# Kernel tuning notes

Measured on AMD Instinct MI355X. Metric: run time of the kernel, lower is better.

The kernel has to match this reference:

```python
import jax, jax.numpy as jnp
import numpy as np

B, S, HID = 2, 2048, 2048
H = 16
HD = HID // H            # 128
HD2 = HD // 2            # 64 (rope dim per head)
LAT = HID // 8           # 256 latent dim
BASE = 10000.0


def _rotary_table(seq_len):
    # inv_freq over rope dim HD2
    inv_freq = 1.0 / (BASE ** (jnp.arange(0, HD2, 2, dtype=jnp.float32) / HD2))  # [HD2//2]
    pos = jnp.arange(seq_len, dtype=jnp.float32)
    sincos = pos[:, None] * inv_freq[None, :]                 # [S, HD2//2]
    return jnp.concatenate([jnp.sin(sincos), jnp.cos(sincos)], axis=-1)  # [S, HD2]


def _apply_rope(x, emb):
    # x: [B, S, H, HD2]; emb: [S, HD2]
    half = HD2 // 2
    x1, x2 = x[..., :half], x[..., half:]
    sin = emb[None, :, None, :half]
    cos = emb[None, :, None, half:]
    return jnp.concatenate([x1 * cos - x2 * sin, x1 * sin + x2 * cos], axis=-1)


def setup_inputs() -> dict:
    key = jax.random.key(0)
    ks = jax.random.split(key, 9)
    s = 0.02
    return {
        "hidden_states": jax.random.normal(ks[0], (B, S, HID), jnp.float32),
        "w_kv_d": jax.random.normal(ks[1], (HID, LAT), jnp.float32) * s,
        "w_q_d": jax.random.normal(ks[2], (HID, LAT), jnp.float32) * s,
        "w_k_u": jax.random.normal(ks[3], (LAT, H * HD2), jnp.float32) * s,
        "w_q_u": jax.random.normal(ks[4], (LAT, H * HD2), jnp.float32) * s,
        "w_v_u": jax.random.normal(ks[5], (LAT, H * HD), jnp.float32) * s,
        "w_rope_k": jax.random.normal(ks[6], (HID, HID // 2), jnp.float32) * s,
        "w_rope_q": jax.random.normal(ks[7], (LAT, HID // 2), jnp.float32) * s,
        "w_o": jax.random.normal(ks[8], (HID, HID), jnp.float32) * s,
    }


def reference(hidden_states, w_kv_d, w_q_d, w_k_u, w_q_u, w_v_u, w_rope_k, w_rope_q, w_o):
    b, s, _ = hidden_states.shape
    kv_d = hidden_states @ w_kv_d            # [B,S,LAT]
    q_d = hidden_states @ w_q_d              # [B,S,LAT]
    k_p = (kv_d @ w_k_u).reshape(b, s, H, HD2)
    q_p = (q_d @ w_q_u).reshape(b, s, H, HD2)
    v = (kv_d @ w_v_u).reshape(b, s, H, HD)
    k_r = (hidden_states @ w_rope_k).reshape(b, s, H, HD2)
    q_r = (q_d @ w_rope_q).reshape(b, s, H, HD2)

    emb = _rotary_table(s)
    k_r = _apply_rope(k_r, emb)
    q_r = _apply_rope(q_r, emb)

    k = jnp.concatenate([k_p, k_r], axis=-1)  # [B,S,H,HD]
    q = jnp.concatenate([q_p, q_r], axis=-1)

    scores = jnp.einsum('bqhd,bkhd->bhqk', q, k) / jnp.sqrt(jnp.float32(HD))
    causal = jnp.tril(jnp.ones((s, s), dtype=bool))
    scores = jnp.where(causal[None, None], scores, jnp.float32(-1e9))
    probs = jax.nn.softmax(scores, axis=-1)
    out = jnp.einsum('bhqk,bkhd->bqhd', probs, v).reshape(b, s, HID)
    return out @ w_o
```

## Files before the change

kernel.cpp:

```cpp
#include <hip/hip_runtime.h>
#include <hip/hip_bf16.h>

#define BB 2
#define SS 2048
#define HID 2048
#define NH 16
#define BS (BB*SS)
#define SCALE 0.088388347648318447f
#define C2LOG 0.12751743f

typedef __bf16 bf16x8 __attribute__((ext_vector_type(8)));
typedef float f32x4 __attribute__((ext_vector_type(4)));
typedef float f32x16 __attribute__((ext_vector_type(16)));
typedef unsigned int uintx2 __attribute__((ext_vector_type(2)));

__device__ __forceinline__ bf16x8 ld_frag(const __hip_bfloat16* p) {
    uint4 u = *reinterpret_cast<const uint4*>(p);
    return __builtin_bit_cast(bf16x8, u);
}
__device__ __forceinline__ void store_c(__hip_bfloat16* C, size_t idx, float v) {
    C[idx] = __float2bfloat16(v);
}
__device__ __forceinline__ void store_c(float* C, size_t idx, float v) {
    C[idx] = v;
}
__device__ __forceinline__ ushort bf_bits(float v) {
    __hip_bfloat16 h = __float2bfloat16(v);
    return *reinterpret_cast<ushort*>(&h);
}

#define GLD16(gp, lp) \
  __builtin_amdgcn_global_load_lds((const __attribute__((address_space(1))) void*)(gp), \
                                   (__attribute__((address_space(3))) void*)(lp), 16, 0, 0)

__global__ __launch_bounds__(256) void convert_kernel(
    const float* __restrict__ src, __hip_bfloat16* __restrict__ dst, int n8)
{
    int i = blockIdx.x * blockDim.x + threadIdx.x;
    if (i >= n8) return;
    float4 a = reinterpret_cast<const float4*>(src)[2 * i];
    float4 b = reinterpret_cast<const float4*>(src)[2 * i + 1];
    ushort u[8] = { bf_bits(a.x), bf_bits(a.y), bf_bits(a.z), bf_bits(a.w),
                    bf_bits(b.x), bf_bits(b.y), bf_bits(b.z), bf_bits(b.w) };
    reinterpret_cast<uint4*>(dst)[i] = *reinterpret_cast<uint4*>(u);
}

__global__ __launch_bounds__(256) void transpose_weights_kernel(
    const float* s0, const float* s1, const float* s2, const float* s3,
    const float* s4, const float* s5, const float* s6, const float* s7,
    __hip_bfloat16* WT1, __hip_bfloat16* WT2, __hip_bfloat16* WT3,
    __hip_bfloat16* WTo)
{
    const float* srcs[8] = { s0, s1, s2, s3, s4, s5, s6, s7 };
    const int Rs[8] = { 2048, 2048, 2048, 256, 256, 256, 256, 2048 };
    const int Cs[8] = { 256, 256, 1024, 1024, 2048, 1024, 1024, 2048 };
    __hip_bfloat16* dsts[8] = {
        WT1, WT1 + (size_t)256 * 2048, WT1 + (size_t)512 * 2048,
        WT2, WT2 + (size_t)1024 * 256,
        WT3, WT3 + (size_t)1024 * 256,
        WTo };
    const int prefix[9] = { 0, 512, 1024, 3072, 3328, 3840, 4096, 4352, 8448 };

    int bid = blockIdx.x;
    int seg = 0;
    #pragma unroll
    for (int i = 0; i < 8; i++) if (bid >= prefix[i + 1]) seg = i + 1;
    int local = bid - prefix[seg];
    int R = Rs[seg], C = Cs[seg];
    int tilesC = C / 32;
    int tr = local / tilesC, tc = local % tilesC;
    int r0 = tr * 32, c0 = tc * 32;
    const float* src = srcs[seg];
    __hip_bfloat16* dst = dsts[seg];

    __shared__ float Ts[32][33];
    int t = threadIdx.x;
    int ty = t >> 5, tx = t & 31;
    #pragma unroll
    for (int k = 0; k < 4; k++) {
        int r = ty + k * 8;
        Ts[r][tx] = src[(size_t)(r0 + r) * C + c0 + tx];
    }
    __syncthreads();
    #pragma unroll
    for (int k = 0; k < 4; k++) {
        int r = ty + k * 8;
        dst[(size_t)(c0 + r) * R + r0 + tx] = __float2bfloat16(Ts[tx][r]);
    }
}

template <typename TC>
__global__ __launch_bounds__(256) void gemm_bt_kernel(
    const __hip_bfloat16* __restrict__ A, int lda,
    const __hip_bfloat16* __restrict__ Bt,
    TC* __restrict__ C0, int ldc0, int sp0, int off0, float cm0,
    TC* __restrict__ C1, int ldc1, int sp1, int off1, float cm1,
    int splitN, int K)
{
    __shared__ alignas(16) __hip_bfloat16 As[128 * 32];
    __shared__ alignas(16) __hip_bfloat16 Bs[128 * 32];

    const int bn = blockIdx.x * 128;
    const int bm = blockIdx.y * 128;
    const int t = threadIdx.x;
    const int w = t >> 6;
    const int lane = t & 63;
    const int l15 = lane & 15;
    const int quad = lane >> 4;
    const int wm = (w & 1) * 64;
    const int wn = (w >> 1) * 64;

    const int srow = lane >> 2;
    const int skcol = (lane & 3) * 8;

    f32x4 acc[4][4] = {};

    for (int k0 = 0; k0 < K; k0 += 32) {
        __syncthreads();
        #pragma unroll
        for (int i = 0; i < 2; i++) {
            int r = w * 32 + i * 16 + srow;
            GLD16(A + (size_t)(bm + r) * lda + k0 + skcol, &As[r * 32 + skcol]);
            GLD16(Bt + (size_t)(bn + r) * K + k0 + skcol, &Bs[r * 32 + skcol]);
        }
        __syncthreads();

        bf16x8 af[4], bf[4];
        #pragma unroll
        for (int mt = 0; mt < 4; mt++)
            af[mt] = ld_frag(&As[(wm + mt * 16 + l15) * 32 + quad * 8]);
        #pragma unroll
        for (int nt = 0; nt < 4; nt++)
            bf[nt] = ld_frag(&Bs[(wn + nt * 16 + l15) * 32 + quad * 8]);
        #pragma unroll
        for (int mt = 0; mt < 4; mt++)
            #pragma unroll
            for (int nt = 0; nt < 4; nt++)
                acc[mt][nt] = __builtin_amdgcn_mfma_f32_16x16x32_bf16(
                    af[mt], bf[nt], acc[mt][nt], 0, 0, 0);
    }

    #pragma unroll
    for (int nt = 0; nt < 4; nt++) {
        int col = bn + wn + nt * 16 + l15;
        TC* Cp; int c, ld, s64, off; float cm;
        if (col < splitN) { Cp = C0; c = col; ld = ldc0; s64 = sp0; off = off0; cm = cm0; }
        else { Cp = C1; c = col - splitN; ld = ldc1; s64 = sp1; off = off1; cm = cm1; }
        if (s64 == 2) {
            #pragma unroll
            for (int mt = 0; mt < 4; mt++) {
                int row0 = bm + wm + mt * 16 + quad * 4;
                #pragma unroll
                for (int r = 0; r < 4; r++)
                    store_c(Cp, (size_t)c * 4096 + row0 + r, acc[mt][nt][r] * cm);
            }
        } else {
            int oc = s64 ? ((c >> 6) * 128 + (c & 63) + off) : c;
            #pragma unroll
            for (int mt = 0; mt < 4; mt++) {
                #pragma unroll
                for (int r = 0; r < 4; r++) {
                    int row = bm + wm + mt * 16 + quad * 4 + r;
                    store_c(Cp, (size_t)row * ld + oc, acc[mt][nt][r] * cm);
                }
            }
        }
    }
}

__global__ __launch_bounds__(256) void rope_kernel(
    __hip_bfloat16* __restrict__ Kb, __hip_bfloat16* __restrict__ Qb)
{
    int idx = blockIdx.x * blockDim.x + threadIdx.x;
    if (idx >= BS * NH * 32) return;
    int i = idx & 31;
    int h = (idx >> 5) & 15;
    int row = idx >> 9;
    int s = row & (SS - 1);

    float inv = exp2f(-(float)i * 0.4152410118609203f);
    float ang = (float)s * inv;
    float sn = sinf(ang), cs = cosf(ang);

    size_t obase = (size_t)row * 2048 + h * 128 + 64 + i;
    {
        float x1 = __bfloat162float(Kb[obase]);
        float x2 = __bfloat162float(Kb[obase + 32]);
        Kb[obase]      = __float2bfloat16(x1 * cs - x2 * sn);
        Kb[obase + 32] = __float2bfloat16(x1 * sn + x2 * cs);
    }
    {
        float x1 = __bfloat162float(Qb[obase]);
        float x2 = __bfloat162float(Qb[obase + 32]);
        Qb[obase]      = __float2bfloat16(x1 * cs - x2 * sn);
        Qb[obase + 32] = __float2bfloat16(x1 * sn + x2 * cs);
    }
}

__global__ __launch_bounds__(256) void flash_attn_kernel(
    const __hip_bfloat16* __restrict__ Q,
    const __hip_bfloat16* __restrict__ Kb,
    const __hip_bfloat16* __restrict__ Vt,
    __hip_bfloat16* __restrict__ O)
{
    __shared__ alignas(16) __hip_bfloat16 Ktd[2 * 4 * 64 * 32];
    __shared__ alignas(16) __hip_bfloat16 Vs[2 * 128 * 32];

    const int bxq = (gridDim.x - 1) - blockIdx.x;
    const int h = blockIdx.y;
    const int b = blockIdx.z;
    const int t = threadIdx.x;
    const int w = t >> 6;
    const int lane = t & 63;
    const int l31 = lane & 31;
    const int hi = lane >> 5;
    const int swl = (l31 >> 1) & 3;
    const int qbase = bxq * 128;
    const int q = qbase + w * 32 + l31;

    const __hip_bfloat16* Kbase = Kb + (size_t)(b * SS) * 2048 + h * 128;
    const __hip_bfloat16* Vtb = Vt + (size_t)(h * 128) * 4096 + b * SS;

    bf16x8 qf[8];
    {
        const __hip_bfloat16* qrow = Q + (size_t)(b * SS + q) * 2048 + h * 128;
        #pragma unroll
        for (int s = 0; s < 8; s++)
            qf[s] = ld_frag(qrow + s * 16 + hi * 8);
    }

    const int Lr = lane >> 2;
    const int Lc = (lane & 3) ^ ((lane >> 3) & 3);
    const int kvh_w = w >> 1, dh_w = w & 1;
    const int ntiles = 2 * bxq + 2;

    float m_i = -INFINITY;
    float l_i = 0.0f;
    f32x16 acc[4] = {};

    #pragma unroll
    for (int i = 0; i < 4; i++)
        GLD16(Kbase + (size_t)(i * 16 + Lr) * 2048 + w * 32 + Lc * 8,
              &Ktd[w * 2048 + i * 512 + lane * 8]);
    asm volatile("" :: "v"(qf[0]), "v"(qf[1]), "v"(qf[2]), "v"(qf[3]),
                       "v"(qf[4]), "v"(qf[5]), "v"(qf[6]), "v"(qf[7]));

    for (int kt = 0; kt < ntiles; kt++) {
        const int kvb = kt * 64;
        const int par = kt & 1;

        __builtin_amdgcn_s_barrier();
        asm volatile("" ::: "memory");

        #pragma unroll
        for (int i = 0; i < 4; i++)
            GLD16(Vtb + (size_t)(dh_w * 64 + i * 16 + Lr) * 4096
                      + kvb + kvh_w * 32 + Lc * 8,
                  &Vs[kvh_w * 4096 + dh_w * 2048 + i * 512 + lane * 8]);
        {
            const int kvb1 = ((kt + 1 < ntiles) ? kt + 1 : ntiles - 1) * 64;
            __hip_bfloat16* kdst = &Ktd[((kt + 1) & 1) * 8192 + w * 2048];
            #pragma unroll
            for (int i = 0; i < 4; i++)
                GLD16(Kbase + (size_t)(kvb1 + i * 16 + Lr) * 2048 + w * 32 + Lc * 8,
                      kdst + i * 512 + lane * 8);
        }
        asm volatile("s_waitcnt vmcnt(8)" ::: "memory");
        __builtin_amdgcn_s_barrier();
        asm volatile("" ::: "memory");

        const __hip_bfloat16* kb_base = &Ktd[par * 8192];
        f32x16 st[2] = {};
        #pragma unroll
        for (int s = 0; s < 8; s++)
            #pragma unroll
            for (int kb = 0; kb < 2; kb++) {
                bf16x8 kf = ld_frag(kb_base + (s >> 1) * 2048 + (kb * 32 + l31) * 32
                                    + ((2 * (s & 1) + hi) ^ swl) * 8);
                st[kb] = __builtin_amdgcn_mfma_f32_32x32x16_bf16(
                    kf, qf[s], st[kb], 0, 0, 0);
            }

        const int thr = q - kvb - 4 * hi;
        float tmx = -INFINITY;
        #pragma unroll
        for (int kb = 0; kb < 2; kb++)
            #pragma unroll
            for (int g = 0; g < 4; g++)
                #pragma unroll
                for (int r = 0; r < 4; r++) {
                    const int e = g * 4 + r;
                    float v = (kb * 32 + 8 * g + r <= thr) ? st[kb][e] : -INFINITY;
                    st[kb][e] = v;
                    tmx = fmaxf(tmx, v);
                }
        tmx = fmaxf(tmx, __shfl_xor(tmx, 32));
        const float m2x = tmx * C2LOG;

        const bool nosc = __all(m2x <= m_i + 8.0f);
        const float mnew = nosc ? m_i : fmaxf(m_i, m2x);
        float rs = 0.0f;
        #pragma unroll
        for (int kb = 0; kb < 2; kb++)
            #pragma unroll
            for (int e = 0; e < 16; e++) {
                float p = exp2f(fmaf(st[kb][e], C2LOG, -mnew));
                st[kb][e] = p;
                rs += p;
            }
        rs += __shfl_xor(rs, 32);
        if (!nosc) {
            const float alpha = exp2f(m_i - mnew);
            m_i = mnew;
            l_i *= alpha;
            #pragma unroll
            for (int dt = 0; dt < 4; dt++)
                #pragma unroll
                for (int e = 0; e < 16; e++)
                    acc[dt][e] *= alpha;
        }
        l_i += rs;

        uint4 af[4];
        #pragma unroll
        for (int kb = 0; kb < 2; kb++) {
            unsigned int pk[4][2];
            #pragma unroll
            for (int g = 0; g < 4; g++)
                #pragma unroll
                for (int i = 0; i < 2; i++) {
                    float2 fp = make_float2(st[kb][g * 4 + 2 * i],
                                            st[kb][g * 4 + 2 * i + 1]);
                    __hip_bfloat162 h2 = __float22bfloat162_rn(fp);
                    pk[g][i] = *reinterpret_cast<unsigned int*>(&h2);
                }
            #pragma unroll
            for (int sl = 0; sl < 2; sl++) {
                uintx2 r0 = __builtin_amdgcn_permlane32_swap(
                    pk[2 * sl][0], pk[2 * sl + 1][0], false, false);
                uintx2 r1 = __builtin_amdgcn_permlane32_swap(
                    pk[2 * sl][1], pk[2 * sl + 1][1], false, false);
                af[kb * 2 + sl] = make_uint4(r0[0], r1[0], r0[1], r1[1]);
            }
        }

        asm volatile("s_waitcnt vmcnt(4)" ::: "memory");
        __builtin_amdgcn_s_barrier();
        asm volatile("" ::: "memory");

        #pragma unroll
        for (int s = 0; s < 4; s++) {
            bf16x8 pf = __builtin_bit_cast(bf16x8, af[s]);
            #pragma unroll
            for (int dt = 0; dt < 4; dt++) {
                bf16x8 vf = ld_frag(&Vs[(s >> 1) * 4096 + (dt * 32 + l31) * 32
                                        + ((2 * (s & 1) + hi) ^ swl) * 8]);
                acc[dt] = __builtin_amdgcn_mfma_f32_32x32x16_bf16(
                    vf, pf, acc[dt], 0, 0, 0);
            }
        }
    }

    const float inv_l = 1.0f / l_i;
    __hip_bfloat16* orow = O + (size_t)(b * SS + q) * 2048 + h * 128;
    #pragma unroll
    for (int dt = 0; dt < 4; dt++)
        #pragma unroll
        for (int g = 0; g < 4; g++) {
            ushort u[4];
            #pragma unroll
            for (int r = 0; r < 4; r++)
                u[r] = bf_bits(acc[dt][g * 4 + r] * inv_l);
            *reinterpret_cast<uint2*>(orow + dt * 32 + 8 * g + 4 * hi) =
                *reinterpret_cast<uint2*>(u);
        }
}

extern "C" void kernel_launch(void* const* d_in, const int* in_sizes, int n_in,
                              void* d_out, int out_size, void* d_ws, size_t ws_size,
                              hipStream_t stream)
{
    const float* hs       = (const float*)d_in[0];
    const float* w_kv_d   = (const float*)d_in[1];
    const float* w_q_d    = (const float*)d_in[2];
    const float* w_k_u    = (const float*)d_in[3];
    const float* w_q_u    = (const float*)d_in[4];
    const float* w_v_u    = (const float*)d_in[5];
    const float* w_rope_k = (const float*)d_in[6];
    const float* w_rope_q = (const float*)d_in[7];
    const float* w_o      = (const float*)d_in[8];
    float* out = (float*)d_out;

    char* p = (char*)d_ws;
    auto alloc = [&](size_t nelem) {
        __hip_bfloat16* r = (__hip_bfloat16*)p;
        p += nelem * sizeof(__hip_bfloat16);
        return r;
    };
    __hip_bfloat16* hsb  = alloc((size_t)BS * HID);
    __hip_bfloat16* qkvd = alloc((size_t)BS * 512);
    __hip_bfloat16* WT1  = alloc((size_t)1536 * 2048);
    __hip_bfloat16* WT2  = alloc((size_t)3072 * 256);
    __hip_bfloat16* WT3  = alloc((size_t)2048 * 256);
    __hip_bfloat16* WTo  = alloc((size_t)2048 * 2048);
    __hip_bfloat16* Kbuf = alloc((size_t)BS * HID);
    __hip_bfloat16* Qbuf = alloc((size_t)BS * HID);
    __hip_bfloat16* Vtb  = alloc((size_t)HID * BS);
    __hip_bfloat16* attn = hsb;

    dim3 blk(256);

    convert_kernel<<<dim3((BS * HID / 8 + 255) / 256), blk, 0, stream>>>(
        hs, hsb, BS * HID / 8);
    transpose_weights_kernel<<<dim3(8448), blk, 0, stream>>>(
        w_kv_d, w_q_d, w_rope_k, w_k_u, w_v_u, w_q_u, w_rope_q, w_o,
        WT1, WT2, WT3, WTo);

    gemm_bt_kernel<__hip_bfloat16><<<dim3(1536 / 128, BS / 128), blk, 0, stream>>>(
        hsb, 2048, WT1,
        qkvd, 512, 0, 0, 1.0f,
        Kbuf, 2048, 1, 64, 1.0f,
        512, 2048);
    gemm_bt_kernel<__hip_bfloat16><<<dim3(3072 / 128, BS / 128), blk, 0, stream>>>(
        qkvd, 512, WT2,
        Kbuf, 2048, 1, 0, 1.0f,
        Vtb, 0, 2, 0, 1.0f,
        1024, 256);
    gemm_bt_kernel<__hip_bfloat16><<<dim3(2048 / 128, BS / 128), blk, 0, stream>>>(
        qkvd + 256, 512, WT3,
        Qbuf, 2048, 1, 0, 1.0f,
        Qbuf, 2048, 1, 64, 1.0f,
        1024, 256);
    rope_kernel<<<dim3((BS * NH * 32 + 255) / 256), blk, 0, stream>>>(Kbuf, Qbuf);
    flash_attn_kernel<<<dim3(SS / 128, NH, BB), blk, 0, stream>>>(
        Qbuf, Kbuf, Vtb, attn);
    gemm_bt_kernel<float><<<dim3(2048 / 128, BS / 128), blk, 0, stream>>>(
        attn, 2048, WTo,
        out, 2048, 0, 0, 1.0f,
        out, 2048, 0, 0, 1.0f,
        2048, 2048);
}
```

Baseline: 371.6 us.

## Pair long and short causal query tiles in one 512-thread attention block

The flash attention kernel now runs 8 waves per block. Waves 0-3 handle query tile 15-p and waves 4-7 handle tile p, so each block does a balanced amount of causal work. K/V tiles loaded into shared memory are shared by both halves, with each wave issuing half as many loads. The grid halves, and waves on the short tile idle through the remaining iterations while still joining the barriers. This aims to remove the causal load imbalance and the per-block tail, at the cost of idle waves and higher per-block register and shared-memory pressure.

After: 360.2 us. 3.1% less time.

```diff
diff --git a/kernel.cpp b/kernel.cpp
--- a/kernel.cpp
+++ b/kernel.cpp
@@ -197,7 +197,7 @@
     }
 }
 
-__global__ __launch_bounds__(256) void flash_attn_kernel(
+__global__ __launch_bounds__(512) void flash_attn_kernel(
     const __hip_bfloat16* __restrict__ Q,
     const __hip_bfloat16* __restrict__ Kb,
     const __hip_bfloat16* __restrict__ Vt,
@@ -206,7 +206,7 @@
     __shared__ alignas(16) __hip_bfloat16 Ktd[2 * 4 * 64 * 32];
     __shared__ alignas(16) __hip_bfloat16 Vs[2 * 128 * 32];
 
-    const int bxq = (gridDim.x - 1) - blockIdx.x;
+    const int p = blockIdx.x;
     const int h = blockIdx.y;
     const int b = blockIdx.z;
     const int t = threadIdx.x;
@@ -215,8 +215,12 @@
     const int l31 = lane & 31;
     const int hi = lane >> 5;
     const int swl = (l31 >> 1) & 3;
-    const int qbase = bxq * 128;
-    const int q = qbase + w * 32 + l31;
+
+    const int qt = (w < 4) ? (15 - p) : p;
+    const int wq = w & 3;
+    const int q = qt * 128 + wq * 32 + l31;
+    const int my_nt = 2 * qt + 2;
+    const int nbig = 2 * (15 - p) + 2;
 
     const __hip_bfloat16* Kbase = Kb + (size_t)(b * SS) * 2048 + h * 128;
     const __hip_bfloat16* Vtb = Vt + (size_t)(h * 128) * 4096 + b * SS;
@@ -231,132 +235,139 @@
 
     const int Lr = lane >> 2;
     const int Lc = (lane & 3) ^ ((lane >> 3) & 3);
-    const int kvh_w = w >> 1, dh_w = w & 1;
-    const int ntiles = 2 * bxq + 2;
 
     float m_i = -INFINITY;
     float l_i = 0.0f;
     f32x16 acc[4] = {};
 
-    #pragma unroll
-    for (int i = 0; i < 4; i++)
-        GLD16(Kbase + (size_t)(i * 16 + Lr) * 2048 + w * 32 + Lc * 8,
-              &Ktd[w * 2048 + i * 512 + lane * 8]);
+    const int kds = w >> 1, khalf = w & 1;
+    const int vkvh = w >> 2, vdq = w & 3;
+
+    #pragma unroll
+    for (int i = 0; i < 2; i++)
+        GLD16(Kbase + (size_t)(khalf * 32 + i * 16 + Lr) * 2048 + kds * 32 + Lc * 8,
+              &Ktd[kds * 2048 + khalf * 1024 + i * 512 + lane * 8]);
     asm volatile("" :: "v"(qf[0]), "v"(qf[1]), "v"(qf[2]), "v"(qf[3]),
                        "v"(qf[4]), "v"(qf[5]), "v"(qf[6]), "v"(qf[7]));
 
-    for (int kt = 0; kt < ntiles; kt++) {
+    for (int kt = 0; kt < nbig; kt++) {
         const int kvb = kt * 64;
         const int par = kt & 1;
+        const bool active = (kt < my_nt);
 
         __builtin_amdgcn_s_barrier();
         asm volatile("" ::: "memory");
 
         #pragma unroll
-        for (int i = 0; i < 4; i++)
-            GLD16(Vtb + (size_t)(dh_w * 64 + i * 16 + Lr) * 4096
-                      + kvb + kvh_w * 32 + Lc * 8,
-                  &Vs[kvh_w * 4096 + dh_w * 2048 + i * 512 + lane * 8]);
+        for (int i = 0; i < 2; i++)
+            GLD16(Vtb + (size_t)(vdq * 32 + i * 16 + Lr) * 4096
+                      + kvb + vkvh * 32 + Lc * 8,
+                  &Vs[vkvh * 4096 + vdq * 1024 + i * 512 + lane * 8]);
         {
-            const int kvb1 = ((kt + 1 < ntiles) ? kt + 1 : ntiles - 1) * 64;
-            __hip_bfloat16* kdst = &Ktd[((kt + 1) & 1) * 8192 + w * 2048];
-            #pragma unroll
-            for (int i = 0; i < 4; i++)
-                GLD16(Kbase + (size_t)(kvb1 + i * 16 + Lr) * 2048 + w * 32 + Lc * 8,
+            const int kvb1 = ((kt + 1 < nbig) ? kt + 1 : nbig - 1) * 64;
+            __hip_bfloat16* kdst = &Ktd[((kt + 1) & 1) * 8192 + kds * 2048 + khalf * 1024];
+            #pragma unroll
+            for (int i = 0; i < 2; i++)
+                GLD16(Kbase + (size_t)(kvb1 + khalf * 32 + i * 16 + Lr) * 2048
+                          + kds * 32 + Lc * 8,
                       kdst + i * 512 + lane * 8);
         }
-        asm volatile("s_waitcnt vmcnt(8)" ::: "memory");
-        __builtin_amdgcn_s_barrier();
-        asm volatile("" ::: "memory");
-
-        const __hip_bfloat16* kb_base = &Ktd[par * 8192];
-        f32x16 st[2] = {};
-        #pragma unroll
-        for (int s = 0; s < 8; s++)
-            #pragma unroll
-            for (int kb = 0; kb < 2; kb++) {
-                bf16x8 kf = ld_frag(kb_base + (s >> 1) * 2048 + (kb * 32 + l31) * 32
-                                    + ((2 * (s & 1) + hi) ^ swl) * 8);
-                st[kb] = __builtin_amdgcn_mfma_f32_32x32x16_bf16(
-                    kf, qf[s], st[kb], 0, 0, 0);
-            }
-
-        const int thr = q - kvb - 4 * hi;
-        float tmx = -INFINITY;
-        #pragma unroll
-        for (int kb = 0; kb < 2; kb++)
-            #pragma unroll
-            for (int g = 0; g < 4; g++)
-                #pragma unroll
-                for (int r = 0; r < 4; r++) {
-                    const int e = g * 4 + r;
-                    float v = (kb * 32 + 8 * g + r <= thr) ? st[kb][e] : -INFINITY;
-                    st[kb][e] = v;
-                    tmx = fmaxf(tmx, v);
-                }
-        tmx = fmaxf(tmx, __shfl_xor(tmx, 32));
-        const float m2x = tmx * C2LOG;
-
-        const bool nosc = __all(m2x <= m_i + 8.0f);
-        const float mnew = nosc ? m_i : fmaxf(m_i, m2x);
-        float rs = 0.0f;
-        #pragma unroll
-        for (int kb = 0; kb < 2; kb++)
-            #pragma unroll
-            for (int e = 0; e < 16; e++) {
-                float p = exp2f(fmaf(st[kb][e], C2LOG, -mnew));
-                st[kb][e] = p;
-                rs += p;
-            }
-        rs += __shfl_xor(rs, 32);
-        if (!nosc) {
-            const float alpha = exp2f(m_i - mnew);
-            m_i = mnew;
-            l_i *= alpha;
-            #pragma unroll
-            for (int dt = 0; dt < 4; dt++)
-                #pragma unroll
-                for (int e = 0; e < 16; e++)
-                    acc[dt][e] *= alpha;
-        }
-        l_i += rs;
-
-        uint4 af[4];
-        #pragma unroll
-        for (int kb = 0; kb < 2; kb++) {
-            unsigned int pk[4][2];
-            #pragma unroll
-            for (int g = 0; g < 4; g++)
-                #pragma unroll
-                for (int i = 0; i < 2; i++) {
-                    float2 fp = make_float2(st[kb][g * 4 + 2 * i],
-                                            st[kb][g * 4 + 2 * i + 1]);
-                    __hip_bfloat162 h2 = __float22bfloat162_rn(fp);
-                    pk[g][i] = *reinterpret_cast<unsigned int*>(&h2);
-                }
-            #pragma unroll
-            for (int sl = 0; sl < 2; sl++) {
-                uintx2 r0 = __builtin_amdgcn_permlane32_swap(
-                    pk[2 * sl][0], pk[2 * sl + 1][0], false, false);
-                uintx2 r1 = __builtin_amdgcn_permlane32_swap(
-                    pk[2 * sl][1], pk[2 * sl + 1][1], false, false);
-                af[kb * 2 + sl] = make_uint4(r0[0], r1[0], r0[1], r1[1]);
-            }
-        }
-
         asm volatile("s_waitcnt vmcnt(4)" ::: "memory");
         __builtin_amdgcn_s_barrier();
         asm volatile("" ::: "memory");
 
-        #pragma unroll
-        for (int s = 0; s < 4; s++) {
-            bf16x8 pf = __builtin_bit_cast(bf16x8, af[s]);
-            #pragma unroll
-            for (int dt = 0; dt < 4; dt++) {
-                bf16x8 vf = ld_frag(&Vs[(s >> 1) * 4096 + (dt * 32 + l31) * 32
-                                        + ((2 * (s & 1) + hi) ^ swl) * 8]);
-                acc[dt] = __builtin_amdgcn_mfma_f32_32x32x16_bf16(
-                    vf, pf, acc[dt], 0, 0, 0);
+        uint4 af[4];
+        if (active) {
+            const __hip_bfloat16* kb_base = &Ktd[par * 8192];
+            f32x16 st[2] = {};
+            #pragma unroll
+            for (int s = 0; s < 8; s++)
+                #pragma unroll
+                for (int kb = 0; kb < 2; kb++) {
+                    bf16x8 kf = ld_frag(kb_base + (s >> 1) * 2048 + (kb * 32 + l31) * 32
+                                        + ((2 * (s & 1) + hi) ^ swl) * 8);
+                    st[kb] = __builtin_amdgcn_mfma_f32_32x32x16_bf16(
+                        kf, qf[s], st[kb], 0, 0, 0);
+                }
+
+            const int thr = q - kvb - 4 * hi;
+            float tmx = -INFINITY;
+            #pragma unroll
+            for (int kb = 0; kb < 2; kb++)
+                #pragma unroll
+                for (int g = 0; g < 4; g++)
+                    #pragma unroll
+                    for (int r = 0; r < 4; r++) {
+                        const int e = g * 4 + r;
+                        float v = (kb * 32 + 8 * g + r <= thr) ? st[kb][e] : -INFINITY;
+                        st[kb][e] = v;
+                        tmx = fmaxf(tmx, v);
+                    }
+            tmx = fmaxf(tmx, __shfl_xor(tmx, 32));
+            const float m2x = tmx * C2LOG;
+
+            const bool nosc = __all(m2x <= m_i + 8.0f);
+            const float mnew = nosc ? m_i : fmaxf(m_i, m2x);
+            float rs = 0.0f;
+            #pragma unroll
+            for (int kb = 0; kb < 2; kb++)
+                #pragma unroll
+                for (int e = 0; e < 16; e++) {
+                    float pv = exp2f(fmaf(st[kb][e], C2LOG, -mnew));
+                    st[kb][e] = pv;
+                    rs += pv;
+                }
+            rs += __shfl_xor(rs, 32);
+            if (!nosc) {
+                const float alpha = exp2f(m_i - mnew);
+                m_i = mnew;
+                l_i *= alpha;
+                #pragma unroll
+                for (int dt = 0; dt < 4; dt++)
+                    #pragma unroll
+                    for (int e = 0; e < 16; e++)
+                        acc[dt][e] *= alpha;
+            }
+            l_i += rs;
+
+            #pragma unroll
+            for (int kb = 0; kb < 2; kb++) {
+                unsigned int pk[4][2];
+                #pragma unroll
+                for (int g = 0; g < 4; g++)
+                    #pragma unroll
+                    for (int i = 0; i < 2; i++) {
+                        float2 fp = make_float2(st[kb][g * 4 + 2 * i],
+                                                st[kb][g * 4 + 2 * i + 1]);
+                        __hip_bfloat162 h2 = __float22bfloat162_rn(fp);
+                        pk[g][i] = *reinterpret_cast<unsigned int*>(&h2);
+                    }
+                #pragma unroll
+                for (int sl = 0; sl < 2; sl++) {
+                    uintx2 r0 = __builtin_amdgcn_permlane32_swap(
+                        pk[2 * sl][0], pk[2 * sl + 1][0], false, false);
+                    uintx2 r1 = __builtin_amdgcn_permlane32_swap(
+                        pk[2 * sl][1], pk[2 * sl + 1][1], false, false);
+                    af[kb * 2 + sl] = make_uint4(r0[0], r1[0], r0[1], r1[1]);
+                }
+            }
+        }
+
+        asm volatile("s_waitcnt vmcnt(2)" ::: "memory");
+        __builtin_amdgcn_s_barrier();
+        asm volatile("" ::: "memory");
+
+        if (active) {
+            #pragma unroll
+            for (int s = 0; s < 4; s++) {
+                bf16x8 pf = __builtin_bit_cast(bf16x8, af[s]);
+                #pragma unroll
+                for (int dt = 0; dt < 4; dt++) {
+                    bf16x8 vf = ld_frag(&Vs[(s >> 1) * 4096 + (dt * 32 + l31) * 32
+                                            + ((2 * (s & 1) + hi) ^ swl) * 8]);
+                    acc[dt] = __builtin_amdgcn_mfma_f32_32x32x16_bf16(
+                        vf, pf, acc[dt], 0, 0, 0);
+                }
             }
         }
     }
@@ -432,7 +443,7 @@
         Qbuf, 2048, 1, 64, 1.0f,
         1024, 256);
     rope_kernel<<<dim3((BS * NH * 32 + 255) / 256), blk, 0, stream>>>(Kbuf, Qbuf);
-    flash_attn_kernel<<<dim3(SS / 128, NH, BB), blk, 0, stream>>>(
+    flash_attn_kernel<<<dim3(8, NH, BB), dim3(512), 0, stream>>>(
         Qbuf, Kbuf, Vtb, attn);
     gemm_bt_kernel<float><<<dim3(2048 / 128, BS / 128), blk, 0, stream>>>(
         attn, 2048, WTo,
```

## Pair complementary causal query tiles per block to balance attention work

Applied to the files above, without the earlier changes.

Each attention block now handles two 64-row query tiles, one from the start and one from the end of the sequence (tiles x and 31-x), so every block does the same total number of KV tiles. Waves whose tile is already finished sit idle while still joining the shared K/V loads and barriers. Masking is skipped for tiles that lie entirely below the diagonal, and MFMA sections are wrapped in s_setprio. The per-block loop now runs to the longer tile's length, so the shorter half of the block idles for part of the loop.

Result: no change. 372.1 us (+0.1%).

```diff
diff --git a/kernel.cpp b/kernel.cpp
--- a/kernel.cpp
+++ b/kernel.cpp
@@ -206,7 +206,7 @@
     __shared__ alignas(16) __hip_bfloat16 Ktd[2 * 4 * 64 * 32];
     __shared__ alignas(16) __hip_bfloat16 Vs[2 * 128 * 32];
 
-    const int bxq = (gridDim.x - 1) - blockIdx.x;
+    const int x = blockIdx.x;
     const int h = blockIdx.y;
     const int b = blockIdx.z;
     const int t = threadIdx.x;
@@ -215,8 +215,12 @@
     const int l31 = lane & 31;
     const int hi = lane >> 5;
     const int swl = (l31 >> 1) & 3;
-    const int qbase = bxq * 128;
-    const int q = qbase + w * 32 + l31;
+
+    const int qt = (w < 2) ? (31 - x) : x;
+    const int qwb = qt * 64 + (w & 1) * 32;
+    const int q = qwb + l31;
+    const int my_nt = qt + 1;
+    const int nbig = 32 - x;
 
     const __hip_bfloat16* Kbase = Kb + (size_t)(b * SS) * 2048 + h * 128;
     const __hip_bfloat16* Vtb = Vt + (size_t)(h * 128) * 4096 + b * SS;
@@ -231,12 +235,12 @@
 
     const int Lr = lane >> 2;
     const int Lc = (lane & 3) ^ ((lane >> 3) & 3);
-    const int kvh_w = w >> 1, dh_w = w & 1;
-    const int ntiles = 2 * bxq + 2;
 
     float m_i = -INFINITY;
     float l_i = 0.0f;
     f32x16 acc[4] = {};
+
+    const int vkvh = w & 1, vdh = w >> 1;
 
     #pragma unroll
     for (int i = 0; i < 4; i++)
@@ -245,20 +249,21 @@
     asm volatile("" :: "v"(qf[0]), "v"(qf[1]), "v"(qf[2]), "v"(qf[3]),
                        "v"(qf[4]), "v"(qf[5]), "v"(qf[6]), "v"(qf[7]));
 
-    for (int kt = 0; kt < ntiles; kt++) {
+    for (int kt = 0; kt < nbig; kt++) {
         const int kvb = kt * 64;
         const int par = kt & 1;
+        const bool active = (kt < my_nt);
 
         __builtin_amdgcn_s_barrier();
         asm volatile("" ::: "memory");
 
         #pragma unroll
         for (int i = 0; i < 4; i++)
-            GLD16(Vtb + (size_t)(dh_w * 64 + i * 16 + Lr) * 4096
-                      + kvb + kvh_w * 32 + Lc * 8,
-                  &Vs[kvh_w * 4096 + dh_w * 2048 + i * 512 + lane * 8]);
+            GLD16(Vtb + (size_t)(vdh * 64 + i * 16 + Lr) * 4096
+                      + kvb + vkvh * 32 + Lc * 8,
+                  &Vs[vkvh * 4096 + vdh * 2048 + i * 512 + lane * 8]);
         {
-            const int kvb1 = ((kt + 1 < ntiles) ? kt + 1 : ntiles - 1) * 64;
+            const int kvb1 = ((kt + 1 < nbig) ? kt + 1 : nbig - 1) * 64;
             __hip_bfloat16* kdst = &Ktd[((kt + 1) & 1) * 8192 + w * 2048];
             #pragma unroll
             for (int i = 0; i < 4; i++)
@@ -269,78 +274,90 @@
         __builtin_amdgcn_s_barrier();
         asm volatile("" ::: "memory");
 
-        const __hip_bfloat16* kb_base = &Ktd[par * 8192];
-        f32x16 st[2] = {};
-        #pragma unroll
-        for (int s = 0; s < 8; s++)
+        uint4 af[4];
+        if (active) {
+            const __hip_bfloat16* kb_base = &Ktd[par * 8192];
+            f32x16 st[2] = {};
+            __builtin_amdgcn_s_setprio(1);
+            #pragma unroll
+            for (int s = 0; s < 8; s++)
+                #pragma unroll
+                for (int kb = 0; kb < 2; kb++) {
+                    bf16x8 kf = ld_frag(kb_base + (s >> 1) * 2048 + (kb * 32 + l31) * 32
+                                        + ((2 * (s & 1) + hi) ^ swl) * 8);
+                    st[kb] = __builtin_amdgcn_mfma_f32_32x32x16_bf16(
+                        kf, qf[s], st[kb], 0, 0, 0);
+                }
+            __builtin_amdgcn_s_setprio(0);
+
+            float tmx = -INFINITY;
+            if (kvb + 63 > qwb) {
+                const int thr = q - kvb - 4 * hi;
+                #pragma unroll
+                for (int kb = 0; kb < 2; kb++)
+                    #pragma unroll
+                    for (int g = 0; g < 4; g++)
+                        #pragma unroll
+                        for (int r = 0; r < 4; r++) {
+                            const int e = g * 4 + r;
+                            float v = (kb * 32 + 8 * g + r <= thr) ? st[kb][e] : -INFINITY;
+                            st[kb][e] = v;
+                            tmx = fmaxf(tmx, v);
+                        }
+            } else {
+                #pragma unroll
+                for (int kb = 0; kb < 2; kb++)
+                    #pragma unroll
+                    for (int e = 0; e < 16; e++)
+                        tmx = fmaxf(tmx, st[kb][e]);
+            }
+            tmx = fmaxf(tmx, __shfl_xor(tmx, 32));
+            const float m2x = tmx * C2LOG;
+
+            const bool nosc = __all(m2x <= m_i + 8.0f);
+            const float mnew = nosc ? m_i : fmaxf(m_i, m2x);
+            float rs = 0.0f;
+            #pragma unroll
+            for (int kb = 0; kb < 2; kb++)
+                #pragma unroll
+                for (int e = 0; e < 16; e++) {
+                    float pv = exp2f(fmaf(st[kb][e], C2LOG, -mnew));
+                    st[kb][e] = pv;
+                    rs += pv;
+                }
+            rs += __shfl_xor(rs, 32);
+            if (!nosc) {
+                const float alpha = exp2f(m_i - mnew);
+                m_i = mnew;
+                l_i *= alpha;
+                #pragma unroll
+                for (int dt = 0; dt < 4; dt++)
+                    #pragma unroll
+                    for (int e = 0; e < 16; e++)
+                        acc[dt][e] *= alpha;
+            }
+            l_i += rs;
+
             #pragma unroll
             for (int kb = 0; kb < 2; kb++) {
-                bf16x8 kf = ld_frag(kb_base + (s >> 1) * 2048 + (kb * 32 + l31) * 32
-                                    + ((2 * (s & 1) + hi) ^ swl) * 8);
-                st[kb] = __builtin_amdgcn_mfma_f32_32x32x16_bf16(
-                    kf, qf[s], st[kb], 0, 0, 0);
-            }
-
-        const int thr = q - kvb - 4 * hi;
-        float tmx = -INFINITY;
-        #pragma unroll
-        for (int kb = 0; kb < 2; kb++)
-            #pragma unroll
-            for (int g = 0; g < 4; g++)
-                #pragma unroll
-                for (int r = 0; r < 4; r++) {
-                    const int e = g * 4 + r;
-                    float v = (kb * 32 + 8 * g + r <= thr) ? st[kb][e] : -INFINITY;
-                    st[kb][e] = v;
-                    tmx = fmaxf(tmx, v);
+                unsigned int pk[4][2];
+                #pragma unroll
+                for (int g = 0; g < 4; g++)
+                    #pragma unroll
+                    for (int i = 0; i < 2; i++) {
+                        float2 fp = make_float2(st[kb][g * 4 + 2 * i],
+                                                st[kb][g * 4 + 2 * i + 1]);
+                        __hip_bfloat162 h2 = __float22bfloat162_rn(fp);
+                        pk[g][i] = *reinterpret_cast<unsigned int*>(&h2);
+                    }
+                #pragma unroll
+                for (int sl = 0; sl < 2; sl++) {
+                    uintx2 r0 = __builtin_amdgcn_permlane32_swap(
+                        pk[2 * sl][0], pk[2 * sl + 1][0], false, false);
+                    uintx2 r1 = __builtin_amdgcn_permlane32_swap(
+                        pk[2 * sl][1], pk[2 * sl + 1][1], false, false);
+                    af[kb * 2 + sl] = make_uint4(r0[0], r1[0], r0[1], r1[1]);
                 }
-        tmx = fmaxf(tmx, __shfl_xor(tmx, 32));
-        const float m2x = tmx * C2LOG;
-
-        const bool nosc = __all(m2x <= m_i + 8.0f);
-        const float mnew = nosc ? m_i : fmaxf(m_i, m2x);
-        float rs = 0.0f;
-        #pragma unroll
-        for (int kb = 0; kb < 2; kb++)
-            #pragma unroll
-            for (int e = 0; e < 16; e++) {
-                float p = exp2f(fmaf(st[kb][e], C2LOG, -mnew));
-                st[kb][e] = p;
-                rs += p;
-            }
-        rs += __shfl_xor(rs, 32);
-        if (!nosc) {
-            const float alpha = exp2f(m_i - mnew);
-            m_i = mnew;
-            l_i *= alpha;
-            #pragma unroll
-            for (int dt = 0; dt < 4; dt++)
-                #pragma unroll
-                for (int e = 0; e < 16; e++)
-                    acc[dt][e] *= alpha;
-        }
-        l_i += rs;
-
-        uint4 af[4];
-        #pragma unroll
-        for (int kb = 0; kb < 2; kb++) {
-            unsigned int pk[4][2];
-            #pragma unroll
-            for (int g = 0; g < 4; g++)
-                #pragma unroll
-                for (int i = 0; i < 2; i++) {
-                    float2 fp = make_float2(st[kb][g * 4 + 2 * i],
-                                            st[kb][g * 4 + 2 * i + 1]);
-                    __hip_bfloat162 h2 = __float22bfloat162_rn(fp);
-                    pk[g][i] = *reinterpret_cast<unsigned int*>(&h2);
-                }
-            #pragma unroll
-            for (int sl = 0; sl < 2; sl++) {
-                uintx2 r0 = __builtin_amdgcn_permlane32_swap(
-                    pk[2 * sl][0], pk[2 * sl + 1][0], false, false);
-                uintx2 r1 = __builtin_amdgcn_permlane32_swap(
-                    pk[2 * sl][1], pk[2 * sl + 1][1], false, false);
-                af[kb * 2 + sl] = make_uint4(r0[0], r1[0], r0[1], r1[1]);
             }
         }
 
@@ -348,16 +365,20 @@
         __builtin_amdgcn_s_barrier();
         asm volatile("" ::: "memory");
 
-        #pragma unroll
-        for (int s = 0; s < 4; s++) {
-            bf16x8 pf = __builtin_bit_cast(bf16x8, af[s]);
-            #pragma unroll
-            for (int dt = 0; dt < 4; dt++) {
-                bf16x8 vf = ld_frag(&Vs[(s >> 1) * 4096 + (dt * 32 + l31) * 32
-                                        + ((2 * (s & 1) + hi) ^ swl) * 8]);
-                acc[dt] = __builtin_amdgcn_mfma_f32_32x32x16_bf16(
-                    vf, pf, acc[dt], 0, 0, 0);
-            }
+        if (active) {
+            __builtin_amdgcn_s_setprio(1);
+            #pragma unroll
+            for (int s = 0; s < 4; s++) {
+                bf16x8 pf = __builtin_bit_cast(bf16x8, af[s]);
+                #pragma unroll
+                for (int dt = 0; dt < 4; dt++) {
+                    bf16x8 vf = ld_frag(&Vs[(s >> 1) * 4096 + (dt * 32 + l31) * 32
+                                            + ((2 * (s & 1) + hi) ^ swl) * 8]);
+                    acc[dt] = __builtin_amdgcn_mfma_f32_32x32x16_bf16(
+                        vf, pf, acc[dt], 0, 0, 0);
+                }
+            }
+            __builtin_amdgcn_s_setprio(0);
         }
     }
 
@@ -432,7 +453,7 @@
         Qbuf, 2048, 1, 64, 1.0f,
         1024, 256);
     rope_kernel<<<dim3((BS * NH * 32 + 255) / 256), blk, 0, stream>>>(Kbuf, Qbuf);
-    flash_attn_kernel<<<dim3(SS / 128, NH, BB), blk, 0, stream>>>(
+    flash_attn_kernel<<<dim3(16, NH, BB), dim3(256), 0, stream>>>(
         Qbuf, Kbuf, Vtb, attn);
     gemm_bt_kernel<float><<<dim3(2048 / 128, BS / 128), blk, 0, stream>>>(
         attn, 2048, WTo,
```
